# Kernel tuning notes

Hardware: AMD Instinct MI355X
Metric: run time of the kernel (lower is better)

Reference implementation:

```python
import jax, jax.numpy as jnp
import numpy as np

N_NODES = 100000

def _sage_conv(h, src, dst, Wl, bl, Wr):
    # PyG SAGEConv (mean aggr): out = lin_l(mean_{j in N(i)} h_j) + lin_r(h_i)
    msg = h[src]                                            # [E, H] gather
    agg = jax.ops.segment_sum(msg, dst, num_segments=N_NODES)   # [N, H] scatter-add
    cnt = jax.ops.segment_sum(jnp.ones((src.shape[0],), h.dtype), dst, num_segments=N_NODES)
    mean = agg / jnp.maximum(cnt, 1.0)[:, None]
    return mean @ Wl + bl + h @ Wr

def setup_inputs() -> dict:
    key = jax.random.key(0)
    ks = jax.random.split(key, 12)
    IN, H, C, E = 256, 128, 40, 1600000
    s = 0.05
    return {
        "x": jax.random.normal(ks[0], (N_NODES, IN), jnp.float32),
        "edge_index": jax.random.randint(ks[1], (2, E), 0, N_NODES, jnp.int32),
        "W_pre": jax.random.normal(ks[2], (IN, H), jnp.float32) * s,
        "b_pre": jnp.zeros((H,), jnp.float32),
        "Wl0": jax.random.normal(ks[3], (H, H), jnp.float32) * s,
        "bl0": jnp.zeros((H,), jnp.float32),
        "Wr0": jax.random.normal(ks[4], (H, H), jnp.float32) * s,
        "Wl1": jax.random.normal(ks[5], (H, H), jnp.float32) * s,
        "bl1": jnp.zeros((H,), jnp.float32),
        "Wr1": jax.random.normal(ks[6], (H, H), jnp.float32) * s,
        "W_post": jax.random.normal(ks[7], (H, C), jnp.float32) * s,
        "b_post": jnp.zeros((C,), jnp.float32),
    }

def reference(x, edge_index, W_pre, b_pre, Wl0, bl0, Wr0, Wl1, bl1, Wr1, W_post, b_post):
    src, dst = edge_index[0], edge_index[1]
    h = x @ W_pre + b_pre                       # pre Linear
    # two SAGEConv layers + relu (dropout is identity in eval mode)
    h = jax.nn.relu(_sage_conv(h, src, dst, Wl0, bl0, Wr0))
    h = jax.nn.relu(_sage_conv(h, src, dst, Wl1, bl1, Wr1))
    logits = h @ W_post + b_post                # post Linear
    return jax.nn.log_softmax(logits, axis=1)
```

## Files before the change

### kernel.cpp

```cpp
#include <hip/hip_runtime.h>
#include <hip/hip_bf16.h>
#include <math.h>

#define N_NODES 100000
#define IN_F 256
#define HID 128
#define NCLS 40

#define NB 782
#define BN 128
#define NC 448
#define CSZ2 3584

typedef __attribute__((ext_vector_type(8))) short short8;
typedef __attribute__((ext_vector_type(4))) float f32x4;

__device__ __forceinline__ short f2bf(float f){
  union { float f; unsigned u; } x; x.f = f;
  unsigned r = (x.u + 0x7fffu + ((x.u >> 16) & 1u)) >> 16;
  return (short)r;
}
__device__ __forceinline__ float bf2f(unsigned short u){
  union { unsigned u; float f; } x; x.u = ((unsigned)u) << 16;
  return x.f;
}

__global__ __launch_bounds__(256) void k_wprep(
    const float* __restrict__ Wpre, const float* __restrict__ Wl0,
    const float* __restrict__ Wr0,  const float* __restrict__ Wl1,
    const float* __restrict__ Wr1,  const float* __restrict__ Wpost,
    unsigned short* __restrict__ img)
{
  const int g = blockIdx.x*256 + threadIdx.x;
  if(g >= 13056) return;
  const int base = g*8;
  unsigned short v[8];
  if(base < 98304){
    const int which = base >> 15;
    const int idx = base & 32767;
    const int l = (idx >> 3) & 63, kb = (idx >> 9) & 7, ct = idx >> 12;
    const int col = ct*16 + (l & 15);
    const float* Wsrc; int kbase;
    if(which == 0){ Wsrc = Wpre; kbase = kb*32 + (l>>4)*8; }
    else{
      Wsrc = (which==1) ? ((kb<4) ? Wl0 : Wr0) : ((kb<4) ? Wl1 : Wr1);
      kbase = (kb&3)*32 + (l>>4)*8;
    }
    #pragma unroll
    for(int j = 0; j < 8; j++) v[j] = (unsigned short)f2bf(Wsrc[(size_t)(kbase+j)*HID + col]);
  } else {
    const int idx = base - 98304;
    const int l = (idx >> 3) & 63, kb = (idx >> 9) & 3, ct = idx >> 11;
    const int col = ct*16 + (l & 15);
    const int kbase = kb*32 + (l>>4)*8;
    #pragma unroll
    for(int j = 0; j < 8; j++)
      v[j] = (col < NCLS) ? (unsigned short)f2bf(Wpost[(size_t)(kbase+j)*NCLS + col]) : 0;
  }
  *reinterpret_cast<short8*>(img + base) = *reinterpret_cast<const short8*>(v);
}

__global__ __launch_bounds__(256) void k_hist(const int* __restrict__ dst, int E,
                                              int* __restrict__ cnt){
  __shared__ int hist[NB];
  const int c = blockIdx.x;
  for(int i = threadIdx.x; i < NB; i += 256) hist[i] = 0;
  __syncthreads();
  const int s0 = c*CSZ2, s1 = min(s0 + CSZ2, E);
  for(int i = s0 + threadIdx.x; i < s1; i += 256)
    atomicAdd(&hist[(unsigned)__builtin_nontemporal_load(dst + i) >> 7], 1);
  __syncthreads();
  for(int i = threadIdx.x; i < NB; i += 256) cnt[c*NB + i] = hist[i];
}

__global__ __launch_bounds__(256) void k_bscanA(const int* __restrict__ cnt,
                                                int* __restrict__ wbase,
                                                int* __restrict__ btot){
  __shared__ int s[256];
  const int b = blockIdx.x;
  const int t = threadIdx.x;
  int v0 = 0, v1 = 0;
  if(2*t < NC)     v0 = cnt[(2*t)*NB + b];
  if(2*t + 1 < NC) v1 = cnt[(2*t+1)*NB + b];
  s[t] = v0 + v1; __syncthreads();
  for(int d = 1; d < 256; d <<= 1){
    int add = (t >= d) ? s[t-d] : 0;
    __syncthreads();
    s[t] += add;
    __syncthreads();
  }
  const int ex = (t > 0) ? s[t-1] : 0;
  if(2*t < NC)     wbase[(2*t)*NB + b] = ex;
  if(2*t + 1 < NC) wbase[(2*t+1)*NB + b] = ex + v0;
  if(t == 255) btot[b] = s[255];
}

__global__ __launch_bounds__(1024) void k_bscanB(const int* __restrict__ btot,
                                                 int* __restrict__ bstart, int E){
  __shared__ int s[1024];
  const int t = threadIdx.x;
  int v = (t < NB) ? btot[t] : 0;
  s[t] = v; __syncthreads();
  for(int d = 1; d < 1024; d <<= 1){
    int add = (t >= d) ? s[t-d] : 0;
    __syncthreads();
    s[t] += add;
    __syncthreads();
  }
  if(t < NB) bstart[t] = s[t] - v;
  if(t == 0) bstart[NB] = E;
}

__global__ __launch_bounds__(256) void k_place(const int* __restrict__ src,
                                               const int* __restrict__ dst, int E,
                                               const int* __restrict__ wbase,
                                               const int* __restrict__ bstart,
                                               int* __restrict__ pk){
  const int g = blockIdx.x;
  const int c = (g & 7)*(NC/8) + (g >> 3);
  __shared__ int cur[NB];
  for(int i = threadIdx.x; i < NB; i += 256)
    cur[i] = wbase[c*NB + i] + bstart[i];
  __syncthreads();
  const int s0 = c*CSZ2, s1 = min(s0 + CSZ2, E);
  for(int i = s0 + threadIdx.x; i < s1; i += 256){
    const int d  = __builtin_nontemporal_load(dst + i);
    const int sv = __builtin_nontemporal_load(src + i);
    const int pos = atomicAdd(&cur[(unsigned)d >> 7], 1);
    pk[pos] = ((d & 127) << 17) | sv;
  }
}

__global__ __launch_bounds__(512) void k_sortb(const int* __restrict__ pk,
                                               const int* __restrict__ bstart,
                                               int* __restrict__ esrc2,
                                               int* __restrict__ nodeoff, int E){
  __shared__ int hist[BN];
  __shared__ int nofs[BN];
  __shared__ int curs[BN];
  const int b = blockIdx.x;
  const int t = threadIdx.x;
  const int bs = bstart[b];
  const int ne = bstart[b+1] - bs;
  for(int i = t; i < BN; i += 512) hist[i] = 0;
  __syncthreads();
  for(int i = t; i < ne; i += 512)
    atomicAdd(&hist[(unsigned)pk[bs + i] >> 17], 1);
  __syncthreads();
  if(t < BN) nofs[t] = hist[t];
  __syncthreads();
  for(int d = 1; d < BN; d <<= 1){
    int add = 0;
    if(t < BN && t >= d) add = nofs[t-d];
    __syncthreads();
    if(t < BN) nofs[t] += add;
    __syncthreads();
  }
  if(t < BN){
    curs[t] = nofs[t] - hist[t];
    const int node = b*BN + t;
    if(node < N_NODES) nodeoff[node] = bs + nofs[t] - hist[t];
    if(node == N_NODES - 1 || (b == NB-1 && t == BN-1)) nodeoff[N_NODES] = E;
  }
  __syncthreads();
  for(int i = t; i < ne; i += 512){
    const int e = pk[bs + i];
    const int pos = atomicAdd(&curs[(unsigned)e >> 17], 1);
    esrc2[bs + pos] = e & 0x1ffff;
  }
}

__global__ __launch_bounds__(256) void k_agg3(
    const unsigned short* __restrict__ h, const int* __restrict__ nodeoff,
    const int* __restrict__ esrc2, unsigned short* __restrict__ mean)
{
  const int lane = threadIdx.x & 63;
  const int wid = blockIdx.x*4 + (threadIdx.x >> 6);
  const int wstride = gridDim.x*4;
  const unsigned* hp = (const unsigned*)h;
  for(int node = wid; node < N_NODES; node += wstride){
    const int beg = nodeoff[node];
    const int deg = nodeoff[node+1] - beg;
    float a0 = 0.f, a1 = 0.f;
    for(int base = 0; base < deg; base += 64){
      const int rem = deg - base;
      const int cnt = rem < 64 ? rem : 64;
      const int myi = (lane < cnt) ? esrc2[beg + base + lane] : 0;
      int e = 0;
      for(; e + 8 <= cnt; e += 8){
        unsigned v[8];
        #pragma unroll
        for(int u = 0; u < 8; u++){
          const int s = __builtin_amdgcn_readlane(myi, e + u);
          v[u] = hp[(size_t)s*64 + lane];
        }
        #pragma unroll
        for(int u = 0; u < 8; u++){
          a0 += bf2f((unsigned short)(v[u] & 0xffffu));
          a1 += bf2f((unsigned short)(v[u] >> 16));
        }
      }
      for(; e < cnt; e++){
        const int s = __builtin_amdgcn_readlane(myi, e);
        const unsigned vv = hp[(size_t)s*64 + lane];
        a0 += bf2f((unsigned short)(vv & 0xffffu));
        a1 += bf2f((unsigned short)(vv >> 16));
      }
    }
    const float inv = (deg > 0) ? (1.0f/(float)deg) : 0.f;
    a0 *= inv; a1 *= inv;
    const unsigned o = ((unsigned)(unsigned short)f2bf(a1) << 16) | (unsigned)(unsigned short)f2bf(a0);
    ((unsigned*)mean)[(size_t)node*64 + lane] = o;
  }
}

__global__ __launch_bounds__(256) void k_gemm_pre(
    const float* __restrict__ x, const unsigned short* __restrict__ wimg,
    const float* __restrict__ b, unsigned short* __restrict__ out)
{
  __shared__ short wlds[8*8*64*8];
  const int t = threadIdx.x;
  {
    short8* dstp = reinterpret_cast<short8*>(wlds);
    const short8* srcp = reinterpret_cast<const short8*>(wimg);
    #pragma unroll
    for(int i = 0; i < 16; i++) dstp[t + i*256] = srcp[t + i*256];
  }
  __syncthreads();
  const int wave = t >> 6, lane = t & 63;
  const int r_in = lane & 15, kg = lane >> 4;
  const int NT = N_NODES/16, stride = gridDim.x*4;

  auto loadx = [&](int tile, float4 (&xa)[8], float4 (&xb)[8]){
    const float* xp = x + (size_t)(tile*16 + r_in)*IN_F + kg*8;
    #pragma unroll
    for(int kb = 0; kb < 8; kb++){
      xa[kb] = *reinterpret_cast<const float4*>(xp + kb*32);
      xb[kb] = *reinterpret_cast<const float4*>(xp + kb*32 + 4);
    }
  };
  auto compute = [&](int tile, const float4 (&xa)[8], const float4 (&xb)[8]){
    f32x4 acc[8];
    #pragma unroll
    for(int ct = 0; ct < 8; ct++) acc[ct] = (f32x4){0.f,0.f,0.f,0.f};
    #pragma unroll
    for(int kb = 0; kb < 8; kb++){
      short8 a;
      a[0]=f2bf(xa[kb].x); a[1]=f2bf(xa[kb].y); a[2]=f2bf(xa[kb].z); a[3]=f2bf(xa[kb].w);
      a[4]=f2bf(xb[kb].x); a[5]=f2bf(xb[kb].y); a[6]=f2bf(xb[kb].z); a[7]=f2bf(xb[kb].w);
      #pragma unroll
      for(int ct = 0; ct < 8; ct++){
        short8 bb = *reinterpret_cast<const short8*>(&wlds[((ct*8+kb)*64+lane)*8]);
        acc[ct] = __builtin_amdgcn_mfma_f32_16x16x32_bf16(a, bb, acc[ct], 0, 0, 0);
      }
    }
    const int row0 = tile*16;
    #pragma unroll
    for(int ct = 0; ct < 8; ct++){
      const int col = ct*16 + r_in;
      const float bias = b[col];
      #pragma unroll
      for(int i = 0; i < 4; i++)
        out[(size_t)(row0 + kg*4 + i)*HID + col] = (unsigned short)f2bf(acc[ct][i] + bias);
    }
  };

  int tile = blockIdx.x*4 + wave;
  if(tile >= NT) return;
  float4 xaA[8], xbA[8], xaB[8], xbB[8];
  loadx(tile, xaA, xbA);
  for(;;){
    int nt = tile + stride;
    bool more = nt < NT;
    if(more) loadx(nt, xaB, xbB);
    compute(tile, xaA, xbA);
    if(!more) break;
    tile = nt;
    nt = tile + stride;
    more = nt < NT;
    if(more) loadx(nt, xaA, xbA);
    compute(tile, xaB, xbB);
    if(!more) break;
    tile = nt;
  }
}

__global__ __launch_bounds__(256) void k_gemm_sage(
    const unsigned short* __restrict__ mean, const unsigned short* __restrict__ h,
    const unsigned short* __restrict__ wimg, const float* __restrict__ bl,
    unsigned short* __restrict__ out)
{
  __shared__ short wlds[8*8*64*8];
  const int t = threadIdx.x;
  {
    short8* dstp = reinterpret_cast<short8*>(wlds);
    const short8* srcp = reinterpret_cast<const short8*>(wimg);
    #pragma unroll
    for(int i = 0; i < 16; i++) dstp[t + i*256] = srcp[t + i*256];
  }
  __syncthreads();
  const int wave = t >> 6, lane = t & 63;
  const int r_in = lane & 15, kg = lane >> 4;
  const int NT = N_NODES/16, stride = gridDim.x*4;

  auto loadx = [&](int tile, short8 (&am)[4], short8 (&ah)[4]){
    const size_t base = (size_t)(tile*16 + r_in)*HID + kg*8;
    #pragma unroll
    for(int kb = 0; kb < 4; kb++){
      am[kb] = *reinterpret_cast<const short8*>(mean + base + kb*32);
      ah[kb] = *reinterpret_cast<const short8*>(h    + base + kb*32);
    }
  };
  auto compute = [&](int tile, const short8 (&am)[4], const short8 (&ah)[4]){
    f32x4 acc[8];
    #pragma unroll
    for(int ct = 0; ct < 8; ct++) acc[ct] = (f32x4){0.f,0.f,0.f,0.f};
    #pragma unroll
    for(int kb = 0; kb < 8; kb++){
      short8 a = (kb < 4) ? am[kb & 3] : ah[kb & 3];
      #pragma unroll
      for(int ct = 0; ct < 8; ct++){
        short8 bb = *reinterpret_cast<const short8*>(&wlds[((ct*8+kb)*64+lane)*8]);
        acc[ct] = __builtin_amdgcn_mfma_f32_16x16x32_bf16(a, bb, acc[ct], 0, 0, 0);
      }
    }
    const int row0 = tile*16;
    #pragma unroll
    for(int ct = 0; ct < 8; ct++){
      const int col = ct*16 + r_in;
      const float bias = bl[col];
      #pragma unroll
      for(int i = 0; i < 4; i++){
        float v = fmaxf(acc[ct][i] + bias, 0.f);
        out[(size_t)(row0 + kg*4 + i)*HID + col] = (unsigned short)f2bf(v);
      }
    }
  };

  int tile = blockIdx.x*4 + wave;
  if(tile >= NT) return;
  short8 amA[4], ahA[4], amB[4], ahB[4];
  loadx(tile, amA, ahA);
  for(;;){
    int nt = tile + stride;
    bool more = nt < NT;
    if(more) loadx(nt, amB, ahB);
    compute(tile, amA, ahA);
    if(!more) break;
    tile = nt;
    nt = tile + stride;
    more = nt < NT;
    if(more) loadx(nt, amA, ahA);
    compute(tile, amB, ahB);
    if(!more) break;
    tile = nt;
  }
}

__global__ __launch_bounds__(256) void k_post(
    const unsigned short* __restrict__ h, const unsigned short* __restrict__ wimg,
    const float* __restrict__ b, float* __restrict__ out)
{
  __shared__ short wlds[3*4*64*8];
  __shared__ float bias_s[48];
  const int t = threadIdx.x;
  {
    short8* dstp = reinterpret_cast<short8*>(wlds);
    const short8* srcp = reinterpret_cast<const short8*>(wimg);
    for(int i = t; i < 768; i += 256) dstp[i] = srcp[i];
  }
  if(t < 48) bias_s[t] = (t < NCLS) ? b[t] : -1e30f;
  __syncthreads();
  const int wave = t >> 6, lane = t & 63;
  const int r_in = lane & 15, kg = lane >> 4;
  for(int tile = blockIdx.x*4 + wave; tile < N_NODES/16; tile += gridDim.x*4){
    const int row0 = tile*16;
    f32x4 acc[3];
    #pragma unroll
    for(int ct = 0; ct < 3; ct++) acc[ct] = (f32x4){0.f,0.f,0.f,0.f};
    #pragma unroll
    for(int kb = 0; kb < 4; kb++){
      short8 a = *reinterpret_cast<const short8*>(h + (size_t)(row0 + r_in)*HID + kb*32 + kg*8);
      #pragma unroll
      for(int ct = 0; ct < 3; ct++){
        short8 bb = *reinterpret_cast<const short8*>(&wlds[((ct*4+kb)*64+lane)*8]);
        acc[ct] = __builtin_amdgcn_mfma_f32_16x16x32_bf16(a, bb, acc[ct], 0, 0, 0);
      }
    }
    #pragma unroll
    for(int i = 0; i < 4; i++){
      float v0 = acc[0][i] + bias_s[r_in];
      float v1 = acc[1][i] + bias_s[16 + r_in];
      float v2 = acc[2][i] + bias_s[32 + r_in];
      float m = fmaxf(fmaxf(v0, v1), v2);
      #pragma unroll
      for(int o = 8; o > 0; o >>= 1) m = fmaxf(m, __shfl_xor(m, o));
      float s = expf(v0 - m) + expf(v1 - m) + expf(v2 - m);
      #pragma unroll
      for(int o = 8; o > 0; o >>= 1) s += __shfl_xor(s, o);
      const float ls = m + logf(s);
      const int row = row0 + kg*4 + i;
      float* op = out + (size_t)row*NCLS;
      op[r_in] = v0 - ls;
      op[16 + r_in] = v1 - ls;
      if(r_in < 8) op[32 + r_in] = v2 - ls;
    }
  }
}

extern "C" void kernel_launch(void* const* d_in, const int* in_sizes, int n_in,
                              void* d_out, int out_size, void* d_ws, size_t ws_size,
                              hipStream_t stream)
{
  const float* x      = (const float*)d_in[0];
  const int*   ei     = (const int*)  d_in[1];
  const float* W_pre  = (const float*)d_in[2];
  const float* b_pre  = (const float*)d_in[3];
  const float* Wl0    = (const float*)d_in[4];
  const float* bl0    = (const float*)d_in[5];
  const float* Wr0    = (const float*)d_in[6];
  const float* Wl1    = (const float*)d_in[7];
  const float* bl1    = (const float*)d_in[8];
  const float* Wr1    = (const float*)d_in[9];
  const float* W_post = (const float*)d_in[10];
  const float* b_post = (const float*)d_in[11];
  float* out = (float*)d_out;

  const int E = in_sizes[1] / 2;
  const int* src = ei;
  const int* dst = ei + E;

  char* ws = (char*)d_ws;
  size_t off = 0;
  auto alloc = [&](size_t bytes)->void*{
    void* p = ws + off;
    off += (bytes + 255) & ~(size_t)255;
    return p;
  };
  unsigned short* hA = (unsigned short*)alloc((size_t)N_NODES*HID*2);
  unsigned short* hB = (unsigned short*)alloc((size_t)N_NODES*HID*2);
  unsigned short* hM = (unsigned short*)alloc((size_t)N_NODES*HID*2);
  int* pk      = (int*)alloc((size_t)E*4);
  int* esrc2   = (int*)alloc((size_t)E*4);
  int* cnt     = (int*)alloc((size_t)NC*NB*4);
  int* wbase   = (int*)alloc((size_t)NC*NB*4);
  int* btot    = (int*)alloc((size_t)NB*4);
  int* bstart  = (int*)alloc((size_t)(NB+1)*4);
  int* nodeoff = (int*)alloc((size_t)(N_NODES+1)*4);
  unsigned short* wimg = (unsigned short*)alloc(104448*2);

  k_wprep<<<51, 256, 0, stream>>>(W_pre, Wl0, Wr0, Wl1, Wr1, W_post, wimg);

  k_hist<<<NC, 256, 0, stream>>>(dst, E, cnt);
  k_bscanA<<<NB, 256, 0, stream>>>(cnt, wbase, btot);
  k_bscanB<<<1, 1024, 0, stream>>>(btot, bstart, E);
  k_place<<<NC, 256, 0, stream>>>(src, dst, E, wbase, bstart, pk);
  k_sortb<<<NB, 512, 0, stream>>>(pk, bstart, esrc2, nodeoff, E);

  k_gemm_pre<<<512, 256, 0, stream>>>(x, wimg, b_pre, hA);

  k_agg3<<<4096, 256, 0, stream>>>(hA, nodeoff, esrc2, hM);
  k_gemm_sage<<<512, 256, 0, stream>>>(hM, hA, wimg + 32768, bl0, hB);

  k_agg3<<<4096, 256, 0, stream>>>(hB, nodeoff, esrc2, hM);
  k_gemm_sage<<<512, 256, 0, stream>>>(hM, hB, wimg + 65536, bl1, hA);

  k_post<<<1563, 256, 0, stream>>>(hA, wimg + 98304, b_post, out);
}
```

Before: 260.3 us.

## Slice edges by source range so aggregation gathers sweep cache-friendly windows

The per-bucket sort now keys edges by destination node and by one of 16 source-ID slices, and writes per-node-per-slice offsets. Each aggregation wave keeps accumulators for 13 nodes and walks the slices in the outer loop. At any moment the whole grid gathers from one narrow band of source rows, which should raise L2 reuse of the random feature gathers. The cost is a 16x larger offset table, more register pressure from the per-node accumulators, a halved grid, and a shorter gather unroll.

```diff
diff --git a/kernel.cpp b/kernel.cpp
--- a/kernel.cpp
+++ b/kernel.cpp
@@ -11,6 +11,8 @@
 #define BN 128
 #define NC 448
 #define CSZ2 3584
+#define NSLICE 16
+#define NPW 13
 
 typedef __attribute__((ext_vector_type(8))) short short8;
 typedef __attribute__((ext_vector_type(4))) float f32x4;
@@ -134,83 +136,108 @@
 __global__ __launch_bounds__(512) void k_sortb(const int* __restrict__ pk,
                                                const int* __restrict__ bstart,
                                                int* __restrict__ esrc2,
-                                               int* __restrict__ nodeoff, int E){
-  __shared__ int hist[BN];
-  __shared__ int nofs[BN];
-  __shared__ int curs[BN];
+                                               int* __restrict__ soff, int E){
+  __shared__ int hist[BN*NSLICE];
+  __shared__ int curs[BN*NSLICE];
+  __shared__ int scn[512];
   const int b = blockIdx.x;
   const int t = threadIdx.x;
   const int bs = bstart[b];
   const int ne = bstart[b+1] - bs;
-  for(int i = t; i < BN; i += 512) hist[i] = 0;
-  __syncthreads();
-  for(int i = t; i < ne; i += 512)
-    atomicAdd(&hist[(unsigned)pk[bs + i] >> 17], 1);
-  __syncthreads();
-  if(t < BN) nofs[t] = hist[t];
-  __syncthreads();
-  for(int d = 1; d < BN; d <<= 1){
-    int add = 0;
-    if(t < BN && t >= d) add = nofs[t-d];
-    __syncthreads();
-    if(t < BN) nofs[t] += add;
-    __syncthreads();
-  }
-  if(t < BN){
-    curs[t] = nofs[t] - hist[t];
-    const int node = b*BN + t;
-    if(node < N_NODES) nodeoff[node] = bs + nofs[t] - hist[t];
-    if(node == N_NODES - 1 || (b == NB-1 && t == BN-1)) nodeoff[N_NODES] = E;
-  }
+  for(int i = t; i < BN*NSLICE; i += 512) hist[i] = 0;
   __syncthreads();
   for(int i = t; i < ne; i += 512){
     const int e = pk[bs + i];
-    const int pos = atomicAdd(&curs[(unsigned)e >> 17], 1);
-    esrc2[bs + pos] = e & 0x1ffff;
-  }
-}
-
-__global__ __launch_bounds__(256) void k_agg3(
-    const unsigned short* __restrict__ h, const int* __restrict__ nodeoff,
+    const int key = ((e >> 17) << 4) | ((e & 0x1ffff) >> 13);
+    atomicAdd(&hist[key], 1);
+  }
+  __syncthreads();
+  const int v0 = hist[4*t], v1 = hist[4*t+1], v2 = hist[4*t+2], v3 = hist[4*t+3];
+  scn[t] = v0 + v1 + v2 + v3; __syncthreads();
+  for(int d = 1; d < 512; d <<= 1){
+    int add = (t >= d) ? scn[t-d] : 0;
+    __syncthreads();
+    scn[t] += add;
+    __syncthreads();
+  }
+  const int ex = (t > 0) ? scn[t-1] : 0;
+  const int st0 = ex, st1 = st0 + v0, st2 = st1 + v1, st3 = st2 + v2;
+  curs[4*t]   = bs + st0;
+  curs[4*t+1] = bs + st1;
+  curs[4*t+2] = bs + st2;
+  curs[4*t+3] = bs + st3;
+  {
+    const int sts[4] = {st0, st1, st2, st3};
+    #pragma unroll
+    for(int j = 0; j < 4; j++){
+      const int key = 4*t + j;
+      const int node = b*BN + (key >> 4);
+      if(node < N_NODES) soff[(size_t)node*NSLICE + (key & 15)] = bs + sts[j];
+    }
+  }
+  if(b == NB-1 && t == 0) soff[(size_t)N_NODES*NSLICE] = E;
+  __syncthreads();
+  for(int i = t; i < ne; i += 512){
+    const int e = pk[bs + i];
+    const int sv = e & 0x1ffff;
+    const int key = ((e >> 17) << 4) | (sv >> 13);
+    const int pos = atomicAdd(&curs[key], 1);
+    esrc2[pos] = sv;
+  }
+}
+
+__global__ __launch_bounds__(256) void k_agg4(
+    const unsigned short* __restrict__ h, const int* __restrict__ soff,
     const int* __restrict__ esrc2, unsigned short* __restrict__ mean)
 {
   const int lane = threadIdx.x & 63;
   const int wid = blockIdx.x*4 + (threadIdx.x >> 6);
   const int wstride = gridDim.x*4;
   const unsigned* hp = (const unsigned*)h;
-  for(int node = wid; node < N_NODES; node += wstride){
-    const int beg = nodeoff[node];
-    const int deg = nodeoff[node+1] - beg;
-    float a0 = 0.f, a1 = 0.f;
-    for(int base = 0; base < deg; base += 64){
-      const int rem = deg - base;
-      const int cnt = rem < 64 ? rem : 64;
-      const int myi = (lane < cnt) ? esrc2[beg + base + lane] : 0;
-      int e = 0;
-      for(; e + 8 <= cnt; e += 8){
-        unsigned v[8];
-        #pragma unroll
-        for(int u = 0; u < 8; u++){
-          const int s = __builtin_amdgcn_readlane(myi, e + u);
-          v[u] = hp[(size_t)s*64 + lane];
-        }
-        #pragma unroll
-        for(int u = 0; u < 8; u++){
-          a0 += bf2f((unsigned short)(v[u] & 0xffffu));
-          a1 += bf2f((unsigned short)(v[u] >> 16));
+  float a0[NPW], a1[NPW];
+  #pragma unroll
+  for(int k = 0; k < NPW; k++){ a0[k] = 0.f; a1[k] = 0.f; }
+  for(int s = 0; s < NSLICE; s++){
+    #pragma unroll
+    for(int k = 0; k < NPW; k++){
+      const int node = wid + k*wstride;
+      if(node < N_NODES){
+        const int beg = soff[(size_t)node*NSLICE + s];
+        const int end = soff[(size_t)node*NSLICE + s + 1];
+        for(int base = beg; base < end; base += 64){
+          const int cnt = min(end - base, 64);
+          const int myi = (lane < cnt) ? esrc2[base + lane] : 0;
+          int e = 0;
+          for(; e + 4 <= cnt; e += 4){
+            unsigned v[4];
+            #pragma unroll
+            for(int u = 0; u < 4; u++)
+              v[u] = hp[(size_t)__builtin_amdgcn_readlane(myi, e + u)*64 + lane];
+            #pragma unroll
+            for(int u = 0; u < 4; u++){
+              a0[k] += bf2f((unsigned short)(v[u] & 0xffffu));
+              a1[k] += bf2f((unsigned short)(v[u] >> 16));
+            }
+          }
+          for(; e < cnt; e++){
+            const unsigned vv = hp[(size_t)__builtin_amdgcn_readlane(myi, e)*64 + lane];
+            a0[k] += bf2f((unsigned short)(vv & 0xffffu));
+            a1[k] += bf2f((unsigned short)(vv >> 16));
+          }
         }
       }
-      for(; e < cnt; e++){
-        const int s = __builtin_amdgcn_readlane(myi, e);
-        const unsigned vv = hp[(size_t)s*64 + lane];
-        a0 += bf2f((unsigned short)(vv & 0xffffu));
-        a1 += bf2f((unsigned short)(vv >> 16));
-      }
-    }
-    const float inv = (deg > 0) ? (1.0f/(float)deg) : 0.f;
-    a0 *= inv; a1 *= inv;
-    const unsigned o = ((unsigned)(unsigned short)f2bf(a1) << 16) | (unsigned)(unsigned short)f2bf(a0);
-    ((unsigned*)mean)[(size_t)node*64 + lane] = o;
+    }
+  }
+  #pragma unroll
+  for(int k = 0; k < NPW; k++){
+    const int node = wid + k*wstride;
+    if(node < N_NODES){
+      const int deg = soff[(size_t)(node+1)*NSLICE] - soff[(size_t)node*NSLICE];
+      const float inv = (deg > 0) ? (1.0f/(float)deg) : 0.f;
+      const float m0 = a0[k]*inv, m1 = a1[k]*inv;
+      const unsigned o = ((unsigned)(unsigned short)f2bf(m1) << 16) | (unsigned)(unsigned short)f2bf(m0);
+      ((unsigned*)mean)[(size_t)node*64 + lane] = o;
+    }
   }
 }
 
@@ -446,7 +473,7 @@
   int* wbase   = (int*)alloc((size_t)NC*NB*4);
   int* btot    = (int*)alloc((size_t)NB*4);
   int* bstart  = (int*)alloc((size_t)(NB+1)*4);
-  int* nodeoff = (int*)alloc((size_t)(N_NODES+1)*4);
+  int* soff    = (int*)alloc(((size_t)N_NODES*NSLICE + 1)*4);
   unsigned short* wimg = (unsigned short*)alloc(104448*2);
 
   k_wprep<<<51, 256, 0, stream>>>(W_pre, Wl0, Wr0, Wl1, Wr1, W_post, wimg);
@@ -455,14 +482,14 @@
   k_bscanA<<<NB, 256, 0, stream>>>(cnt, wbase, btot);
   k_bscanB<<<1, 1024, 0, stream>>>(btot, bstart, E);
   k_place<<<NC, 256, 0, stream>>>(src, dst, E, wbase, bstart, pk);
-  k_sortb<<<NB, 512, 0, stream>>>(pk, bstart, esrc2, nodeoff, E);
+  k_sortb<<<NB, 512, 0, stream>>>(pk, bstart, esrc2, soff, E);
 
   k_gemm_pre<<<512, 256, 0, stream>>>(x, wimg, b_pre, hA);
 
-  k_agg3<<<4096, 256, 0, stream>>>(hA, nodeoff, esrc2, hM);
+  k_agg4<<<2048, 256, 0, stream>>>(hA, soff, esrc2, hM);
   k_gemm_sage<<<512, 256, 0, stream>>>(hM, hA, wimg + 32768, bl0, hB);
 
-  k_agg3<<<4096, 256, 0, stream>>>(hB, nodeoff, esrc2, hM);
+  k_agg4<<<2048, 256, 0, stream>>>(hB, soff, esrc2, hM);
   k_gemm_sage<<<512, 256, 0, stream>>>(hM, hB, wimg + 65536, bl1, hA);
 
   k_post<<<1563, 256, 0, stream>>>(hA, wimg + 98304, b_post, out);
```

Measured after the change: 734.0 us. +182.0%, slower.
